# Optimization experiments

Measured on AMD Instinct MI355X. Metric: run time of the kernel, lower is better.

Reference implementation:

```python
import jax, jax.numpy as jnp
import numpy as np

B = 4096        # batch_size
H = 512         # hidden_rep_dim
S = 16384       # codebook_size (sae_dim)
K = 32          # opt.k (live topk per sample, applied batch-wise)
DEAD_K = 16     # opt.dead_k
DEAD_THRESH = 5


def setup_inputs() -> dict:
    key = jax.random.key(0)
    k0, k1, k2, k3 = jax.random.split(key, 4)
    x = jax.random.normal(k0, (B, H), dtype=jnp.float32)
    W1 = jax.random.normal(k1, (S, H), dtype=jnp.float32) * 0.02
    b1 = jnp.zeros((S,), dtype=jnp.float32)
    W2 = jax.random.normal(k2, (H, S), dtype=jnp.float32) * 0.02
    b2 = jnp.zeros((H,), dtype=jnp.float32)
    dead_features = jax.random.randint(k3, (S,), 0, 10, dtype=jnp.int32)
    return {"x": x, "W1": W1, "b1": b1, "W2": W2, "b2": b2,
            "dead_features": dead_features}


def reference(x, W1, b1, W2, b2, dead_features):
    Bn = x.shape[0]
    # _x = x - sae2.bias; f = relu(sae1(_x))
    f = jax.nn.relu((x - b2) @ W1.T + b1)          # [B, S]
    f_flat = f.reshape(-1)                          # [B*S]

    # batch topk over the flattened activations
    topk_vals, topk_inds = jax.lax.top_k(f_flat, K * Bn)

    # dead-feature masked activations; topk over them.
    # torch uses n = min(num_dead_slots, DEAD_K*B); taking a fixed DEAD_K*B topk
    # is value-equivalent since extra picks are zeros scattered onto zeros.
    dead_mask = (dead_features >= DEAD_THRESH)      # [S]
    dead_f_flat = jnp.where(
        jnp.broadcast_to(dead_mask[None, :], f.shape).reshape(-1),
        f_flat, jnp.zeros((), f.dtype))
    dead_vals, dead_inds = jax.lax.top_k(dead_f_flat, DEAD_K * Bn)

    # scatter kept values into zeroed tensors, unflatten
    f_sparse = jnp.zeros_like(f_flat).at[topk_inds].set(topk_vals).reshape(Bn, -1)
    dead_sparse = jnp.zeros_like(f_flat).at[dead_inds].set(dead_vals).reshape(Bn, -1)

    # dual decode through sae2
    x_rec = f_sparse @ W2.T + b2                    # [B, H]
    dead_x = dead_sparse @ W2.T + b2                # [B, H]
    return (x_rec, f_sparse, dead_x)
```

## Files before the change

### kernel.cpp

```cpp
#include <hip/hip_runtime.h>
#include <stdint.h>

#define B_  4096
#define H_  512
#define S_  16384
#define KT_ 16
#define NEED_MAIN 131072
#define NEED_DEAD 65536
#define DEAD_THRESH 5

#define T_LO 1.05078125f
#define BIN_BASE 0x3F800000u
#define BIN_SHIFT 13
#define NBIN 2048
#define REG_W 8
#define PAD_BINS 2
#define NSUB 8192
#define TIECAP 512

#define NSEG 16384
#define CAPSEG_M 128
#define CAPSEG_D 64
#define BNDCAP 16384
#define CAPROW_M 192
#define CAPROW_D 128

typedef __bf16 bf16x8 __attribute__((ext_vector_type(8)));
typedef float f32x4 __attribute__((ext_vector_type(4)));
typedef unsigned short ushort8 __attribute__((ext_vector_type(8)));

__device__ __forceinline__ uint32_t binOf(float v) {
    uint32_t b = (__float_as_uint(v) - BIN_BASE) >> BIN_SHIFT;
    return b > (NBIN - 1) ? (NBIN - 1) : b;
}
__device__ __forceinline__ uint16_t f2bf(float f) {
    uint32_t u = __float_as_uint(f);
    uint32_t r = u + 0x7FFFu + ((u >> 16) & 1u);
    return (uint16_t)(r >> 16);
}
__device__ __forceinline__ float bf2f(uint16_t b) {
    return __uint_as_float((uint32_t)b << 16);
}
__device__ __forceinline__ void gload16(const void* g, void* l) {
    __builtin_amdgcn_global_load_lds((const __attribute__((address_space(1))) uint32_t*)g,
                                     (__attribute__((address_space(3))) uint32_t*)l, 16, 0, 0);
}

__global__ __launch_bounds__(256) void transpose_k(const float* __restrict__ W2,
                                                   uint16_t* __restrict__ W2T) {
    __shared__ float tile[32][33];
    int s0 = blockIdx.x * 32, h0 = blockIdx.y * 32;
    int tx = threadIdx.x & 31, ty = threadIdx.x >> 5;
#pragma unroll
    for (int i = 0; i < 4; i++) {
        int h = h0 + ty + i * 8;
        tile[ty + i * 8][tx] = W2[(size_t)h * S_ + s0 + tx];
    }
    __syncthreads();
#pragma unroll
    for (int i = 0; i < 4; i++) {
        int s = s0 + ty + i * 8;
        W2T[(size_t)s * H_ + h0 + tx] = f2bf(tile[tx][ty + i * 8]);
    }
}

__global__ __launch_bounds__(256) void split_k(const float* __restrict__ src,
                                               const float* __restrict__ sub,
                                               uint8_t* __restrict__ Th,
                                               uint8_t* __restrict__ Tl) {
    int tid = blockIdx.x * 256 + threadIdx.x;
    int r = tid >> 6, h8 = tid & 63;
    int k0 = h8 << 3;
    const float* s = src + (size_t)r * H_ + k0;
    float4 v0 = *(const float4*)s, v1 = *(const float4*)(s + 4);
    float a[8] = {v0.x, v0.y, v0.z, v0.w, v1.x, v1.y, v1.z, v1.w};
    if (sub) {
        float4 c0 = *(const float4*)(sub + k0), c1 = *(const float4*)(sub + k0 + 4);
        a[0] -= c0.x; a[1] -= c0.y; a[2] -= c0.z; a[3] -= c0.w;
        a[4] -= c1.x; a[5] -= c1.y; a[6] -= c1.z; a[7] -= c1.w;
    }
    ushort8 Hh, Ll;
#pragma unroll
    for (int e = 0; e < 8; e++) {
        uint16_t h = f2bf(a[e]);
        Hh[e] = h;
        Ll[e] = f2bf(a[e] - bf2f(h));
    }
    int rb = r >> 7, kt = k0 >> 5;
    int mf = (r >> 4) & 7;
    int ln = (r & 15) | (((k0 >> 3) & 3) << 4);
    size_t byte = ((size_t)rb * KT_ + kt) * 8192 + (size_t)mf * 1024 + (size_t)ln * 16;
    *(ushort8*)(Th + byte) = Hh;
    if (Tl) *(ushort8*)(Tl + byte) = Ll;
}

__global__ __launch_bounds__(256) void gemm_fused(const uint8_t* __restrict__ AhT,
                                                  const uint8_t* __restrict__ AlT,
                                                  const uint8_t* __restrict__ WhT,
                                                  const float* __restrict__ b1,
                                                  const int* __restrict__ deadf,
                                                  uint2* __restrict__ glM,
                                                  uint2* __restrict__ glD,
                                                  uint32_t* __restrict__ bcM,
                                                  uint32_t* __restrict__ bcD,
                                                  float* __restrict__ fsp) {
    __shared__ uint8_t lds[2][3][8192];
    const int tid = threadIdx.x;
    const int lane = tid & 63, w = tid >> 6;
    const int wr = w >> 1, wc = w & 1;
    const int lin = blockIdx.y * 512 + blockIdx.x;
    const int xcd = lin & 7, idx = lin >> 3;
    const int mb = xcd * 4 + (idx & 3), nb = idx >> 2;

    const uint8_t* gAh = AhT + (size_t)mb * KT_ * 8192;
    const uint8_t* gAl = AlT + (size_t)mb * KT_ * 8192;
    const uint8_t* gBh = WhT + (size_t)nb * KT_ * 8192;

    f32x4 acc[4][4];
#pragma unroll
    for (int i = 0; i < 4; i++)
#pragma unroll
        for (int j = 0; j < 4; j++) acc[i][j] = (f32x4){0.f, 0.f, 0.f, 0.f};

    auto stage = [&](int buf, int kt) {
        size_t tb = (size_t)kt * 8192;
#pragma unroll
        for (int j = 0; j < 2; j++) {
            int off = j * 4096 + tid * 16;
            gload16(gAh + tb + off, &lds[buf][0][off]);
            gload16(gAl + tb + off, &lds[buf][1][off]);
            gload16(gBh + tb + off, &lds[buf][2][off]);
        }
    };

    float* Fb = fsp + (size_t)(mb * 128) * S_ + nb * 128;
    const int zc4 = (tid & 31) * 4, zr0 = tid >> 5;
    const float4 zf4 = {0.f, 0.f, 0.f, 0.f};

    stage(0, 0);
    __syncthreads();
    for (int kt = 0; kt < KT_; kt++) {
        int cur = kt & 1;
        if (kt + 1 < KT_) stage(cur ^ 1, kt + 1);
        *(float4*)(Fb + (size_t)(zr0 + kt * 8) * S_ + zc4) = zf4;
        bf16x8 ah[4], al[4], bh[4];
#pragma unroll
        for (int i = 0; i < 4; i++) {
            int offA = (wr * 4 + i) * 1024 + lane * 16;
            int offB = (wc * 4 + i) * 1024 + lane * 16;
            ah[i] = *(const bf16x8*)&lds[cur][0][offA];
            al[i] = *(const bf16x8*)&lds[cur][1][offA];
            bh[i] = *(const bf16x8*)&lds[cur][2][offB];
        }
#pragma unroll
        for (int i = 0; i < 4; i++)
#pragma unroll
            for (int j = 0; j < 4; j++)
                acc[i][j] = __builtin_amdgcn_mfma_f32_16x16x32_bf16(ah[i], bh[j], acc[i][j], 0, 0, 0);
#pragma unroll
        for (int i = 0; i < 4; i++)
#pragma unroll
            for (int j = 0; j < 4; j++)
                acc[i][j] = __builtin_amdgcn_mfma_f32_16x16x32_bf16(al[i], bh[j], acc[i][j], 0, 0, 0);
        __syncthreads();
    }

    const int col0 = nb * 128 + wc * 64 + (lane & 15);
    const int row0 = mb * 128 + wr * 64 + (lane >> 4) * 4;
    float b1v[4];
    int dd[4];
#pragma unroll
    for (int j = 0; j < 4; j++) {
        b1v[j] = b1[col0 + j * 16];
        dd[j] = (deadf[col0 + j * 16] >= DEAD_THRESH) ? 1 : 0;
    }
    const uint32_t gseg = (uint32_t)(mb * 128 + nb) * 4 + w;
    uint2* segM = glM + (size_t)gseg * CAPSEG_M;
    uint2* segD = glD + (size_t)gseg * CAPSEG_D;
    const uint64_t lmlt = ((uint64_t)1 << lane) - 1;
    uint32_t runM = 0, runD = 0;
#pragma unroll
    for (int i = 0; i < 4; i++)
#pragma unroll
        for (int j = 0; j < 4; j++)
#pragma unroll
            for (int r = 0; r < 4; r++) {
                float v = fmaxf(acc[i][j][r] + b1v[j], 0.0f);
                bool pass = v >= T_LO;
                uint64_t mask = __ballot(pass);
                if (mask) {
                    uint32_t prefix = (uint32_t)__popcll(mask & lmlt);
                    uint2 ent;
                    ent.x = (uint32_t)(row0 + i * 16 + r) * S_ + (uint32_t)(col0 + j * 16);
                    ent.y = __float_as_uint(v);
                    if (pass && runM + prefix < CAPSEG_M) segM[runM + prefix] = ent;
                    runM += (uint32_t)__popcll(mask);
                    bool dp = pass && dd[j];
                    uint64_t dmask = __ballot(dp);
                    if (dmask) {
                        uint32_t dprefix = (uint32_t)__popcll(dmask & lmlt);
                        if (dp && runD + dprefix < CAPSEG_D) segD[runD + dprefix] = ent;
                        runD += (uint32_t)__popcll(dmask);
                    }
                }
            }
    if (lane == 0) {
        bcM[gseg] = runM < CAPSEG_M ? runM : CAPSEG_M;
        bcD[gseg] = runD < CAPSEG_D ? runD : CAPSEG_D;
    }
}

__global__ __launch_bounds__(256) void seg_scan_k(const uint32_t* __restrict__ bcM,
                                                  const uint32_t* __restrict__ bcD,
                                                  uint32_t* __restrict__ soM,
                                                  uint32_t* __restrict__ soD,
                                                  uint32_t* __restrict__ cnts) {
    __shared__ uint32_t part[256];
    const int t = threadIdx.x;
    for (int sel = 0; sel < 2; sel++) {
        const uint32_t* bc = sel ? bcD : bcM;
        uint32_t* so = sel ? soD : soM;
        uint32_t s = 0;
        for (int i = 0; i < NSEG / 256; i++) s += bc[t * (NSEG / 256) + i];
        part[t] = s;
        __syncthreads();
        for (int d = 1; d < 256; d <<= 1) {
            uint32_t v = (t >= d) ? part[t - d] : 0;
            __syncthreads();
            part[t] += v;
            __syncthreads();
        }
        uint32_t run = (t == 0) ? 0 : part[t - 1];
        for (int i = 0; i < NSEG / 256; i++) {
            uint32_t c = bc[t * (NSEG / 256) + i];
            so[t * (NSEG / 256) + i] = run;
            run += c;
        }
        if (t == 255) cnts[sel] = run;
        __syncthreads();
    }
}

__global__ __launch_bounds__(256) void compact_hist_k(const uint2* __restrict__ glM,
                                                      const uint2* __restrict__ glD,
                                                      const uint32_t* __restrict__ bcM,
                                                      const uint32_t* __restrict__ bcD,
                                                      const uint32_t* __restrict__ soM,
                                                      const uint32_t* __restrict__ soD,
                                                      uint2* __restrict__ cmpM,
                                                      uint2* __restrict__ cmpD,
                                                      uint32_t* __restrict__ ghM,
                                                      uint32_t* __restrict__ ghD) {
    __shared__ uint32_t h[NBIN];
    int sel = blockIdx.y;
    const uint2* list = sel ? glD : glM;
    const uint32_t* bc = sel ? bcD : bcM;
    const uint32_t* so = sel ? soD : soM;
    uint2* cmp = sel ? cmpD : cmpM;
    uint32_t cap = sel ? CAPSEG_D : CAPSEG_M;
    uint32_t* gh = sel ? ghD : ghM;
    for (int i = threadIdx.x; i < NBIN; i += 256) h[i] = 0;
    __syncthreads();
    const int wv = threadIdx.x >> 6, lane = threadIdx.x & 63;
    for (uint32_t seg = blockIdx.x * 4 + wv; seg < NSEG; seg += gridDim.x * 4) {
        uint32_t n = bc[seg], off = so[seg];
        for (uint32_t i = lane; i < n; i += 64) {
            uint2 e = list[(size_t)seg * cap + i];
            cmp[off + i] = e;
            atomicAdd(&h[binOf(__uint_as_float(e.y))], 1u);
        }
    }
    __syncthreads();
    for (int i = threadIdx.x; i < NBIN; i += 256)
        if (h[i]) atomicAdd(&gh[i], h[i]);
}

__global__ __launch_bounds__(256) void scan_k(const uint32_t* __restrict__ ghM,
                                              const uint32_t* __restrict__ ghD,
                                              uint32_t* __restrict__ scal) {
    __shared__ uint32_t h[NBIN];
    __shared__ uint32_t csum[64];
    for (int sel = 0; sel < 2; sel++) {
        const uint32_t* gh = sel ? ghD : ghM;
        uint32_t need = sel ? NEED_DEAD : NEED_MAIN;
        for (int i = threadIdx.x; i < NBIN; i += 256) h[i] = gh[i];
        __syncthreads();
        if (threadIdx.x < 64) {
            uint32_t s = 0;
#pragma unroll
            for (int j = 0; j < 32; j++) s += h[threadIdx.x * 32 + j];
            csum[threadIdx.x] = s;
        }
        __syncthreads();
        if (threadIdx.x == 0) {
            uint32_t cum = 0; int c = 63;
            for (; c > 0; c--) { uint32_t cc = csum[c]; if (cum + cc >= need) break; cum += cc; }
            int b = c * 32 + 31;
            for (; b > c * 32; b--) { uint32_t cc = h[b]; if (cum + cc >= need) break; cum += cc; }
            uint32_t extra = 0;
            for (int j = b + 1; j < b + REG_W && j < NBIN; j++) extra += h[j];
            scal[sel ? 2 : 0] = (uint32_t)b;
            scal[sel ? 3 : 1] = need - cum + extra;
        }
        __syncthreads();
    }
}

__global__ __launch_bounds__(256) void bnd_filter_k(const uint2* __restrict__ cmpM,
                                                    const uint2* __restrict__ cmpD,
                                                    const uint32_t* __restrict__ scal,
                                                    uint2* __restrict__ bndM,
                                                    uint2* __restrict__ bndD,
                                                    uint32_t* __restrict__ cnts) {
    int sel = blockIdx.y;
    const uint2* list = sel ? cmpD : cmpM;
    uint2* bnd = sel ? bndD : bndM;
    uint32_t n = cnts[sel];
    uint32_t bs = scal[sel ? 2 : 0];
    for (uint32_t i = blockIdx.x * 256 + threadIdx.x; i < n; i += gridDim.x * 256) {
        uint2 ent = list[i];
        uint32_t bb = binOf(__uint_as_float(ent.y));
        if (bb + REG_W >= bs && bb <= bs + REG_W - 1) {
            uint32_t p = atomicAdd(&cnts[2 + sel], 1u);
            if (p < BNDCAP) bnd[p] = ent;
        }
    }
}

__global__ __launch_bounds__(256) void bnd_f64_k(const uint2* __restrict__ bndM,
                                                 const uint2* __restrict__ bndD,
                                                 const uint32_t* __restrict__ cnts,
                                                 const float* __restrict__ x,
                                                 const float* __restrict__ w1,
                                                 const float* __restrict__ b1,
                                                 const float* __restrict__ b2,
                                                 double* __restrict__ bvM,
                                                 double* __restrict__ bvD) {
    int sel = blockIdx.y;
    const uint2* bnd = sel ? bndD : bndM;
    double* bv64 = sel ? bvD : bvM;
    uint32_t n = cnts[2 + sel]; if (n > BNDCAP) n = BNDCAP;
    uint32_t i = blockIdx.x * 4 + (threadIdx.x >> 6);
    if (i >= n) return;
    const int lane = threadIdx.x & 63;
    uint2 ent = bnd[i];
    uint32_t m = ent.x >> 14, s = ent.x & (S_ - 1);
    const float* xr = x + (size_t)m * H_;
    const float* wr = w1 + (size_t)s * H_;
    double sum = 0.0;
#pragma unroll
    for (int e = 0; e < 8; e++) {
        int k = lane + e * 64;
        sum += ((double)xr[k] - (double)b2[k]) * (double)wr[k];
    }
#pragma unroll
    for (int off = 32; off; off >>= 1) sum += __shfl_down(sum, off, 64);
    if (lane == 0) {
        double tot = sum + (double)b1[s];
        bv64[i] = tot > 0.0 ? tot : 0.0;
    }
}

__global__ __launch_bounds__(1024) void rank_hist_k(const uint2* __restrict__ bndM,
                                                    const double* __restrict__ bvM,
                                                    const uint2* __restrict__ bndD,
                                                    const double* __restrict__ bvD,
                                                    uint32_t* __restrict__ cnts,
                                                    const uint32_t* __restrict__ scal,
                                                    uint2* __restrict__ exM,
                                                    uint2* __restrict__ exD) {
    int sel = blockIdx.x;
    const uint2* bnd = sel ? bndD : bndM;
    const double* bv = sel ? bvD : bvM;
    uint2* ex = sel ? exD : exM;
    uint32_t n = cnts[2 + sel]; if (n > BNDCAP) n = BNDCAP;
    uint32_t r = scal[sel ? 3 : 1]; if (r > n) r = n;
    uint32_t bs = scal[sel ? 2 : 0];
    uint32_t loBin = bs - (REG_W + PAD_BINS);
    uint32_t hiBin = bs + (REG_W + PAD_BINS);
    double lo = (double)__uint_as_float(BIN_BASE + (loBin << BIN_SHIFT));
    double hi = (double)__uint_as_float(BIN_BASE + (hiBin << BIN_SHIFT));
    double scale = (double)NSUB / (hi - lo);

    __shared__ uint32_t h[NSUB];
    __shared__ uint32_t cs[1024];
    __shared__ uint32_t c2[64];
    __shared__ uint32_t sCb, sAbove, sExPos, sTieCnt;
    __shared__ double tieV[TIECAP];
    __shared__ uint2 tieE[TIECAP];
    const int t = threadIdx.x;
    for (int i = t; i < NSUB; i += 1024) h[i] = 0;
    if (t == 0) { sExPos = 0; sTieCnt = 0; }
    __syncthreads();
    for (uint32_t i = t; i < n; i += 1024) {
        double v = bv[i];
        int k = (int)((v - lo) * scale);
        k = k < 0 ? 0 : (k > NSUB - 1 ? NSUB - 1 : k);
        atomicAdd(&h[k], 1u);
    }
    __syncthreads();
    {
        uint32_t s = 0;
#pragma unroll
        for (int j = 0; j < 8; j++) s += h[t * 8 + j];
        cs[t] = s;
    }
    __syncthreads();
    if (t < 64) {
        uint32_t s = 0;
#pragma unroll
        for (int j = 0; j < 16; j++) s += cs[t * 16 + j];
        c2[t] = s;
    }
    __syncthreads();
    if (t == 0) {
        uint32_t cum = 0; int w2 = 63;
        for (; w2 > 0; w2--) { if (cum + c2[w2] >= r) break; cum += c2[w2]; }
        int c = w2 * 16 + 15;
        for (; c > w2 * 16; c--) { if (cum + cs[c] >= r) break; cum += cs[c]; }
        int b = c * 8 + 7;
        for (; b > c * 8; b--) { if (cum + h[b] >= r) break; cum += h[b]; }
        sCb = (uint32_t)b;
        sAbove = cum;
    }
    __syncthreads();
    const uint32_t cb = sCb;
    uint32_t rr = r - sAbove;
    const int lane = t & 63;
    const uint64_t lmlt = ((uint64_t)1 << lane) - 1;
    for (uint32_t i0 = 0; i0 < n; i0 += 1024) {
        uint32_t i = i0 + t;
        bool valid = i < n;
        double v = valid ? bv[i] : -1.0;
        uint32_t k = 0;
        if (valid) {
            int kk = (int)((v - lo) * scale);
            k = (uint32_t)(kk < 0 ? 0 : (kk > NSUB - 1 ? NSUB - 1 : kk));
        }
        bool pick = valid && k > cb;
        uint64_t m = __ballot(pick);
        if (m) {
            uint32_t base = 0;
            if (lane == 0) base = atomicAdd(&sExPos, (uint32_t)__popcll(m));
            base = __shfl(base, 0, 64);
            if (pick) ex[base + __popcll(m & lmlt)] = bnd[i];
        }
        bool tie = valid && k == cb;
        uint64_t tm = __ballot(tie);
        if (tm) {
            uint32_t base = 0;
            if (lane == 0) base = atomicAdd(&sTieCnt, (uint32_t)__popcll(tm));
            base = __shfl(base, 0, 64);
            if (tie) {
                uint32_t p = base + __popcll(tm & lmlt);
                if (p < TIECAP) { tieV[p] = v; tieE[p] = bnd[i]; }
            }
        }
    }
    __syncthreads();
    uint32_t tc = sTieCnt; if (tc > TIECAP) tc = TIECAP;
    if (rr > tc) rr = tc;
    if (t < (int)tc) {
        double vi = tieV[t]; uint32_t ii = tieE[t].x;
        uint32_t rank = 0;
        for (uint32_t j = 0; j < tc; j++) {
            double vj = tieV[j]; uint32_t ij = tieE[j].x;
            rank += (vj > vi || (vj == vi && ij < ii)) ? 1u : 0u;
        }
        if (rank < rr) {
            uint32_t p = atomicAdd(&sExPos, 1u);
            ex[p] = tieE[t];
        }
    }
    __syncthreads();
    if (t == 0) cnts[4 + sel] = sExPos;
}

__global__ __launch_bounds__(256) void scatter_list_k(const uint2* __restrict__ cmpM,
                                                      const uint2* __restrict__ cmpD,
                                                      const uint32_t* __restrict__ cnts,
                                                      const uint32_t* __restrict__ scal,
                                                      float* __restrict__ fsp,
                                                      uint2* __restrict__ entM,
                                                      uint2* __restrict__ entD,
                                                      uint32_t* __restrict__ rcM,
                                                      uint32_t* __restrict__ rcD) {
    int sel = blockIdx.y;
    const uint2* list = sel ? cmpD : cmpM;
    uint2* entries = sel ? entD : entM;
    uint32_t* rowCnt = sel ? rcD : rcM;
    int capRow = sel ? CAPROW_D : CAPROW_M;
    uint32_t n = cnts[sel];
    uint32_t bsReg = scal[sel ? 2 : 0] + REG_W - 1;
    for (uint32_t i = blockIdx.x * 256 + threadIdx.x; i < n; i += gridDim.x * 256) {
        uint2 ent = list[i];
        float v = __uint_as_float(ent.y);
        if (binOf(v) <= bsReg) continue;
        if (!sel) fsp[ent.x] = v;
        uint32_t row = ent.x >> 14;
        uint32_t slot = atomicAdd(&rowCnt[row], 1u);
        if (slot < (uint32_t)capRow)
            entries[(size_t)row * capRow + slot] = make_uint2(ent.x & (S_ - 1), ent.y);
    }
}

__global__ __launch_bounds__(256) void scatter_ex_k(const uint2* __restrict__ exM,
                                                    const uint2* __restrict__ exD,
                                                    const uint32_t* __restrict__ cnts,
                                                    float* __restrict__ fsp,
                                                    uint2* __restrict__ entM,
                                                    uint2* __restrict__ entD,
                                                    uint32_t* __restrict__ rcM,
                                                    uint32_t* __restrict__ rcD) {
    int sel = blockIdx.y;
    const uint2* arr = sel ? exD : exM;
    uint2* entries = sel ? entD : entM;
    uint32_t* rowCnt = sel ? rcD : rcM;
    int capRow = sel ? CAPROW_D : CAPROW_M;
    uint32_t n = cnts[4 + sel]; if (n > BNDCAP) n = BNDCAP;
    uint32_t i = blockIdx.x * 256 + threadIdx.x;
    if (i >= n) return;
    uint2 ent = arr[i];
    float v = __uint_as_float(ent.y);
    if (!sel) fsp[ent.x] = v;
    uint32_t row = ent.x >> 14;
    uint32_t slot = atomicAdd(&rowCnt[row], 1u);
    if (slot < (uint32_t)capRow)
        entries[(size_t)row * capRow + slot] = make_uint2(ent.x & (S_ - 1), ent.y);
}

__global__ __launch_bounds__(512) void decode_k(const uint2* __restrict__ entM,
                                                const uint32_t* __restrict__ rcM,
                                                const uint2* __restrict__ entD,
                                                const uint32_t* __restrict__ rcD,
                                                const uint16_t* __restrict__ W2T,
                                                const float* __restrict__ b2,
                                                float* __restrict__ xrec,
                                                float* __restrict__ deadx) {
    __shared__ uint2 em[CAPROW_M];
    __shared__ uint2 ed[CAPROW_D];
    int b = blockIdx.x, h = threadIdx.x;
    uint32_t nm = rcM[b]; if (nm > CAPROW_M) nm = CAPROW_M;
    uint32_t nd = rcD[b]; if (nd > CAPROW_D) nd = CAPROW_D;
    for (uint32_t i = h; i < nm; i += 512) em[i] = entM[(size_t)b * CAPROW_M + i];
    for (uint32_t i = h; i < nd; i += 512) ed[i] = entD[(size_t)b * CAPROW_D + i];
    __syncthreads();
    float bias = b2[h];
    float a = bias, d = bias;
    for (uint32_t i = 0; i < nm; i++)
        a = fmaf(__uint_as_float(em[i].y), bf2f(W2T[(size_t)em[i].x * H_ + h]), a);
    for (uint32_t i = 0; i < nd; i++)
        d = fmaf(__uint_as_float(ed[i].y), bf2f(W2T[(size_t)ed[i].x * H_ + h]), d);
    xrec[(size_t)b * H_ + h] = a;
    deadx[(size_t)b * H_ + h] = d;
}

extern "C" void kernel_launch(void* const* d_in, const int* in_sizes, int n_in,
                              void* d_out, int out_size, void* d_ws, size_t ws_size,
                              hipStream_t stream) {
    const float* x = (const float*)d_in[0];
    const float* w1 = (const float*)d_in[1];
    const float* b1 = (const float*)d_in[2];
    const float* w2 = (const float*)d_in[3];
    const float* b2 = (const float*)d_in[4];
    const int* deadf = (const int*)d_in[5];

    float* out = (float*)d_out;
    float* xrec = out;
    float* fsp = out + (size_t)B_ * H_;
    float* deadx = out + (size_t)B_ * H_ + (size_t)B_ * S_;

    uint8_t* w = (uint8_t*)d_ws;
    size_t off = 0;
    auto alloc = [&](size_t bytes) { uint8_t* p = w + off; off = (off + bytes + 255) & ~(size_t)255; return p; };

    uint16_t* W2T = (uint16_t*)alloc((size_t)S_ * H_ * 2);
    uint8_t* ctrl = alloc(NBIN * 8 + 128 + (size_t)B_ * 8);
    uint32_t* ghM = (uint32_t*)ctrl;
    uint32_t* ghD = (uint32_t*)(ctrl + NBIN * 4);
    uint32_t* cnts = (uint32_t*)(ctrl + NBIN * 8);
    uint32_t* scal = (uint32_t*)(ctrl + NBIN * 8 + 64);
    uint32_t* rcM = (uint32_t*)(ctrl + NBIN * 8 + 128);
    uint32_t* rcD = (uint32_t*)(ctrl + NBIN * 8 + 128 + B_ * 4);
    size_t ctrlBytes = NBIN * 8 + 128 + (size_t)B_ * 8;

    uint2* listM = (uint2*)alloc((size_t)NSEG * CAPSEG_M * 8);
    uint2* listD = (uint2*)alloc((size_t)NSEG * CAPSEG_D * 8);
    uint32_t* bcM = (uint32_t*)alloc((size_t)NSEG * 4);
    uint32_t* bcD = (uint32_t*)alloc((size_t)NSEG * 4);
    uint32_t* soM = (uint32_t*)alloc((size_t)NSEG * 4);
    uint32_t* soD = (uint32_t*)alloc((size_t)NSEG * 4);
    uint2* cmpM = (uint2*)alloc((size_t)NSEG * CAPSEG_M * 8);
    uint2* cmpD = (uint2*)alloc((size_t)NSEG * CAPSEG_D * 8);
    uint2* bndM = (uint2*)alloc((size_t)BNDCAP * 8);
    uint2* bndD = (uint2*)alloc((size_t)BNDCAP * 8);
    double* bvM = (double*)alloc((size_t)BNDCAP * 8);
    double* bvD = (double*)alloc((size_t)BNDCAP * 8);
    uint2* exM = (uint2*)alloc((size_t)BNDCAP * 8);
    uint2* exD = (uint2*)alloc((size_t)BNDCAP * 8);
    uint2* entM = (uint2*)alloc((size_t)B_ * CAPROW_M * 8);
    uint2* entD = (uint2*)alloc((size_t)B_ * CAPROW_D * 8);
    uint8_t* AhT = alloc((size_t)B_ * H_ * 2);
    uint8_t* AlT = alloc((size_t)B_ * H_ * 2);
    uint8_t* WhT = alloc((size_t)S_ * H_ * 2);

    (void)hipMemsetAsync(ctrl, 0, ctrlBytes, stream);
    transpose_k<<<dim3(S_ / 32, H_ / 32), 256, 0, stream>>>(w2, W2T);
    split_k<<<(B_ * 64) / 256, 256, 0, stream>>>(x, b2, AhT, AlT);
    split_k<<<(S_ * 64) / 256, 256, 0, stream>>>(w1, nullptr, WhT, nullptr);
    gemm_fused<<<dim3(512, 8), 256, 0, stream>>>(AhT, AlT, WhT, b1, deadf,
                                                 listM, listD, bcM, bcD, fsp);
    seg_scan_k<<<1, 256, 0, stream>>>(bcM, bcD, soM, soD, cnts);
    compact_hist_k<<<dim3(256, 2), 256, 0, stream>>>(listM, listD, bcM, bcD, soM, soD,
                                                     cmpM, cmpD, ghM, ghD);
    scan_k<<<1, 256, 0, stream>>>(ghM, ghD, scal);
    bnd_filter_k<<<dim3(1024, 2), 256, 0, stream>>>(cmpM, cmpD, scal, bndM, bndD, cnts);
    bnd_f64_k<<<dim3(BNDCAP / 4, 2), 256, 0, stream>>>(bndM, bndD, cnts, x, w1, b1, b2, bvM, bvD);
    rank_hist_k<<<2, 1024, 0, stream>>>(bndM, bvM, bndD, bvD, cnts, scal, exM, exD);
    scatter_list_k<<<dim3(1024, 2), 256, 0, stream>>>(cmpM, cmpD, cnts, scal, fsp,
                                                      entM, entD, rcM, rcD);
    scatter_ex_k<<<dim3(BNDCAP / 256, 2), 256, 0, stream>>>(exM, exD, cnts, fsp, entM, entD, rcM, rcD);
    decode_k<<<B_, 512, 0, stream>>>(entM, rcM, entD, rcD, W2T, b2, xrec, deadx);
}
```

Before: 494.1 us.

## Fuse split, boundary filter/f64, and exact scatter kernels; widen GEMM to 8 waves

Merges the two split launches into one grid, fuses the boundary filter with the fp64 recompute, and folds the exact-tie scatter into rank_hist so the ex buffers and the scatter_ex launch go away. The GEMM block grows to 512 threads with each wave covering a 64x32 sub-tile, which doubles the number of per-wave candidate segments (NSEG raised to match). The intent is fewer launches and more waves for latency hiding. The cost is fewer accumulators per wave, less register-level reuse of the A fragments, and fp64 work done serially per wave inside the ballot loop.

```diff
diff --git a/kernel.cpp b/kernel.cpp
--- a/kernel.cpp
+++ b/kernel.cpp
@@ -18,7 +18,7 @@
 #define NSUB 8192
 #define TIECAP 512
 
-#define NSEG 16384
+#define NSEG 32768
 #define CAPSEG_M 128
 #define CAPSEG_D 64
 #define BNDCAP 16384
@@ -64,18 +64,22 @@
     }
 }
 
-__global__ __launch_bounds__(256) void split_k(const float* __restrict__ src,
-                                               const float* __restrict__ sub,
-                                               uint8_t* __restrict__ Th,
-                                               uint8_t* __restrict__ Tl) {
-    int tid = blockIdx.x * 256 + threadIdx.x;
+__global__ __launch_bounds__(256) void split_all_k(const float* __restrict__ x,
+                                                   const float* __restrict__ w1,
+                                                   const float* __restrict__ b2,
+                                                   uint8_t* __restrict__ AhT,
+                                                   uint8_t* __restrict__ AlT,
+                                                   uint8_t* __restrict__ WhT) {
+    int isX = blockIdx.x < 1024;
+    int tid = (isX ? blockIdx.x : blockIdx.x - 1024) * 256 + threadIdx.x;
     int r = tid >> 6, h8 = tid & 63;
     int k0 = h8 << 3;
+    const float* src = isX ? x : w1;
     const float* s = src + (size_t)r * H_ + k0;
     float4 v0 = *(const float4*)s, v1 = *(const float4*)(s + 4);
     float a[8] = {v0.x, v0.y, v0.z, v0.w, v1.x, v1.y, v1.z, v1.w};
-    if (sub) {
-        float4 c0 = *(const float4*)(sub + k0), c1 = *(const float4*)(sub + k0 + 4);
+    if (isX) {
+        float4 c0 = *(const float4*)(b2 + k0), c1 = *(const float4*)(b2 + k0 + 4);
         a[0] -= c0.x; a[1] -= c0.y; a[2] -= c0.z; a[3] -= c0.w;
         a[4] -= c1.x; a[5] -= c1.y; a[6] -= c1.z; a[7] -= c1.w;
     }
@@ -90,11 +94,15 @@
     int mf = (r >> 4) & 7;
     int ln = (r & 15) | (((k0 >> 3) & 3) << 4);
     size_t byte = ((size_t)rb * KT_ + kt) * 8192 + (size_t)mf * 1024 + (size_t)ln * 16;
-    *(ushort8*)(Th + byte) = Hh;
-    if (Tl) *(ushort8*)(Tl + byte) = Ll;
-}
-
-__global__ __launch_bounds__(256) void gemm_fused(const uint8_t* __restrict__ AhT,
+    if (isX) {
+        *(ushort8*)(AhT + byte) = Hh;
+        *(ushort8*)(AlT + byte) = Ll;
+    } else {
+        *(ushort8*)(WhT + byte) = Hh;
+    }
+}
+
+__global__ __launch_bounds__(512) void gemm_fused(const uint8_t* __restrict__ AhT,
                                                   const uint8_t* __restrict__ AlT,
                                                   const uint8_t* __restrict__ WhT,
                                                   const float* __restrict__ b1,
@@ -107,7 +115,7 @@
     __shared__ uint8_t lds[2][3][8192];
     const int tid = threadIdx.x;
     const int lane = tid & 63, w = tid >> 6;
-    const int wr = w >> 1, wc = w & 1;
+    const int wr = w >> 2, wc = w & 3;
     const int lin = blockIdx.y * 512 + blockIdx.x;
     const int xcd = lin & 7, idx = lin >> 3;
     const int mb = xcd * 4 + (idx & 3), nb = idx >> 2;
@@ -116,21 +124,18 @@
     const uint8_t* gAl = AlT + (size_t)mb * KT_ * 8192;
     const uint8_t* gBh = WhT + (size_t)nb * KT_ * 8192;
 
-    f32x4 acc[4][4];
+    f32x4 acc[4][2];
 #pragma unroll
     for (int i = 0; i < 4; i++)
 #pragma unroll
-        for (int j = 0; j < 4; j++) acc[i][j] = (f32x4){0.f, 0.f, 0.f, 0.f};
+        for (int j = 0; j < 2; j++) acc[i][j] = (f32x4){0.f, 0.f, 0.f, 0.f};
 
     auto stage = [&](int buf, int kt) {
         size_t tb = (size_t)kt * 8192;
-#pragma unroll
-        for (int j = 0; j < 2; j++) {
-            int off = j * 4096 + tid * 16;
-            gload16(gAh + tb + off, &lds[buf][0][off]);
-            gload16(gAl + tb + off, &lds[buf][1][off]);
-            gload16(gBh + tb + off, &lds[buf][2][off]);
-        }
+        int o = tid * 16;
+        gload16(gAh + tb + o, &lds[buf][0][o]);
+        gload16(gAl + tb + o, &lds[buf][1][o]);
+        gload16(gBh + tb + o, &lds[buf][2][o]);
     };
 
     float* Fb = fsp + (size_t)(mb * 128) * S_ + nb * 128;
@@ -142,39 +147,42 @@
     for (int kt = 0; kt < KT_; kt++) {
         int cur = kt & 1;
         if (kt + 1 < KT_) stage(cur ^ 1, kt + 1);
-        *(float4*)(Fb + (size_t)(zr0 + kt * 8) * S_ + zc4) = zf4;
-        bf16x8 ah[4], al[4], bh[4];
+        if (kt < 8) *(float4*)(Fb + (size_t)(zr0 + kt * 16) * S_ + zc4) = zf4;
+        bf16x8 ah[4], al[4], bh[2];
 #pragma unroll
         for (int i = 0; i < 4; i++) {
             int offA = (wr * 4 + i) * 1024 + lane * 16;
-            int offB = (wc * 4 + i) * 1024 + lane * 16;
             ah[i] = *(const bf16x8*)&lds[cur][0][offA];
             al[i] = *(const bf16x8*)&lds[cur][1][offA];
-            bh[i] = *(const bf16x8*)&lds[cur][2][offB];
+        }
+#pragma unroll
+        for (int j = 0; j < 2; j++) {
+            int offB = (wc * 2 + j) * 1024 + lane * 16;
+            bh[j] = *(const bf16x8*)&lds[cur][2][offB];
         }
 #pragma unroll
         for (int i = 0; i < 4; i++)
 #pragma unroll
-            for (int j = 0; j < 4; j++)
+            for (int j = 0; j < 2; j++)
                 acc[i][j] = __builtin_amdgcn_mfma_f32_16x16x32_bf16(ah[i], bh[j], acc[i][j], 0, 0, 0);
 #pragma unroll
         for (int i = 0; i < 4; i++)
 #pragma unroll
-            for (int j = 0; j < 4; j++)
+            for (int j = 0; j < 2; j++)
                 acc[i][j] = __builtin_amdgcn_mfma_f32_16x16x32_bf16(al[i], bh[j], acc[i][j], 0, 0, 0);
         __syncthreads();
     }
 
-    const int col0 = nb * 128 + wc * 64 + (lane & 15);
+    const int col0 = nb * 128 + wc * 32 + (lane & 15);
     const int row0 = mb * 128 + wr * 64 + (lane >> 4) * 4;
-    float b1v[4];
-    int dd[4];
-#pragma unroll
-    for (int j = 0; j < 4; j++) {
+    float b1v[2];
+    int dd[2];
+#pragma unroll
+    for (int j = 0; j < 2; j++) {
         b1v[j] = b1[col0 + j * 16];
         dd[j] = (deadf[col0 + j * 16] >= DEAD_THRESH) ? 1 : 0;
     }
-    const uint32_t gseg = (uint32_t)(mb * 128 + nb) * 4 + w;
+    const uint32_t gseg = (uint32_t)(mb * 128 + nb) * 8 + w;
     uint2* segM = glM + (size_t)gseg * CAPSEG_M;
     uint2* segD = glD + (size_t)gseg * CAPSEG_D;
     const uint64_t lmlt = ((uint64_t)1 << lane) - 1;
@@ -182,7 +190,7 @@
 #pragma unroll
     for (int i = 0; i < 4; i++)
 #pragma unroll
-        for (int j = 0; j < 4; j++)
+        for (int j = 0; j < 2; j++)
 #pragma unroll
             for (int r = 0; r < 4; r++) {
                 float v = fmaxf(acc[i][j][r] + b1v[j], 0.0f);
@@ -306,58 +314,62 @@
     }
 }
 
-__global__ __launch_bounds__(256) void bnd_filter_k(const uint2* __restrict__ cmpM,
-                                                    const uint2* __restrict__ cmpD,
-                                                    const uint32_t* __restrict__ scal,
-                                                    uint2* __restrict__ bndM,
-                                                    uint2* __restrict__ bndD,
-                                                    uint32_t* __restrict__ cnts) {
+__global__ __launch_bounds__(256) void bnd_fused_k(const uint2* __restrict__ cmpM,
+                                                   const uint2* __restrict__ cmpD,
+                                                   const uint32_t* __restrict__ scal,
+                                                   const float* __restrict__ x,
+                                                   const float* __restrict__ w1,
+                                                   const float* __restrict__ b1,
+                                                   const float* __restrict__ b2,
+                                                   uint2* __restrict__ bndM,
+                                                   uint2* __restrict__ bndD,
+                                                   double* __restrict__ bvM,
+                                                   double* __restrict__ bvD,
+                                                   uint32_t* __restrict__ cnts) {
     int sel = blockIdx.y;
     const uint2* list = sel ? cmpD : cmpM;
     uint2* bnd = sel ? bndD : bndM;
+    double* bv64 = sel ? bvD : bvM;
     uint32_t n = cnts[sel];
     uint32_t bs = scal[sel ? 2 : 0];
-    for (uint32_t i = blockIdx.x * 256 + threadIdx.x; i < n; i += gridDim.x * 256) {
-        uint2 ent = list[i];
-        uint32_t bb = binOf(__uint_as_float(ent.y));
-        if (bb + REG_W >= bs && bb <= bs + REG_W - 1) {
-            uint32_t p = atomicAdd(&cnts[2 + sel], 1u);
-            if (p < BNDCAP) bnd[p] = ent;
-        }
-    }
-}
-
-__global__ __launch_bounds__(256) void bnd_f64_k(const uint2* __restrict__ bndM,
-                                                 const uint2* __restrict__ bndD,
-                                                 const uint32_t* __restrict__ cnts,
-                                                 const float* __restrict__ x,
-                                                 const float* __restrict__ w1,
-                                                 const float* __restrict__ b1,
-                                                 const float* __restrict__ b2,
-                                                 double* __restrict__ bvM,
-                                                 double* __restrict__ bvD) {
-    int sel = blockIdx.y;
-    const uint2* bnd = sel ? bndD : bndM;
-    double* bv64 = sel ? bvD : bvM;
-    uint32_t n = cnts[2 + sel]; if (n > BNDCAP) n = BNDCAP;
-    uint32_t i = blockIdx.x * 4 + (threadIdx.x >> 6);
-    if (i >= n) return;
-    const int lane = threadIdx.x & 63;
-    uint2 ent = bnd[i];
-    uint32_t m = ent.x >> 14, s = ent.x & (S_ - 1);
-    const float* xr = x + (size_t)m * H_;
-    const float* wr = w1 + (size_t)s * H_;
-    double sum = 0.0;
-#pragma unroll
-    for (int e = 0; e < 8; e++) {
-        int k = lane + e * 64;
-        sum += ((double)xr[k] - (double)b2[k]) * (double)wr[k];
-    }
-#pragma unroll
-    for (int off = 32; off; off >>= 1) sum += __shfl_down(sum, off, 64);
-    if (lane == 0) {
-        double tot = sum + (double)b1[s];
-        bv64[i] = tot > 0.0 ? tot : 0.0;
+    const int lane = threadIdx.x & 63, wv = threadIdx.x >> 6;
+    const uint32_t stride = gridDim.x * 4 * 64;
+    for (uint32_t base = (blockIdx.x * 4 + wv) * 64; base < n; base += stride) {
+        uint32_t i = base + lane;
+        uint2 ent = make_uint2(0u, 0u);
+        bool pass = false;
+        if (i < n) {
+            ent = list[i];
+            uint32_t bb = binOf(__uint_as_float(ent.y));
+            pass = (bb + REG_W >= bs) && (bb <= bs + REG_W - 1);
+        }
+        uint64_t mm = __ballot(pass);
+        while (mm) {
+            int b = __ffsll((unsigned long long)mm) - 1;
+            mm &= mm - 1;
+            uint32_t ex_ = __shfl(ent.x, b, 64);
+            uint32_t ey_ = __shfl(ent.y, b, 64);
+            uint32_t pos = 0;
+            if (lane == 0) pos = atomicAdd(&cnts[2 + sel], 1u);
+            pos = __shfl(pos, 0, 64);
+            if (pos >= BNDCAP) continue;
+            uint32_t m = ex_ >> 14, s = ex_ & (S_ - 1);
+            const float* xr = x + (size_t)m * H_;
+            const float* wr = w1 + (size_t)s * H_;
+            double sum = 0.0;
+#pragma unroll
+            for (int e = 0; e < 8; e++) {
+                int k = lane + e * 64;
+                sum += ((double)xr[k] - (double)b2[k]) * (double)wr[k];
+            }
+#pragma unroll
+            for (int off = 32; off; off >>= 1) sum += __shfl_down(sum, off, 64);
+            if (lane == 0) {
+                double tot = sum + (double)b1[s];
+                bv64[pos] = tot > 0.0 ? tot : 0.0;
+                bnd[pos] = make_uint2(ex_, ey_);
+            }
+        }
     }
 }
 
@@ -367,12 +379,17 @@
                                                     const double* __restrict__ bvD,
                                                     uint32_t* __restrict__ cnts,
                                                     const uint32_t* __restrict__ scal,
-                                                    uint2* __restrict__ exM,
-                                                    uint2* __restrict__ exD) {
+                                                    float* __restrict__ fsp,
+                                                    uint2* __restrict__ entM,
+                                                    uint2* __restrict__ entD,
+                                                    uint32_t* __restrict__ rcM,
+                                                    uint32_t* __restrict__ rcD) {
     int sel = blockIdx.x;
     const uint2* bnd = sel ? bndD : bndM;
     const double* bv = sel ? bvD : bvM;
-    uint2* ex = sel ? exD : exM;
+    uint2* entries = sel ? entD : entM;
+    uint32_t* rowCnt = sel ? rcD : rcM;
+    const int capRow = sel ? CAPROW_D : CAPROW_M;
     uint32_t n = cnts[2 + sel]; if (n > BNDCAP) n = BNDCAP;
     uint32_t r = scal[sel ? 3 : 1]; if (r > n) r = n;
     uint32_t bs = scal[sel ? 2 : 0];
@@ -385,12 +402,12 @@
     __shared__ uint32_t h[NSUB];
     __shared__ uint32_t cs[1024];
     __shared__ uint32_t c2[64];
-    __shared__ uint32_t sCb, sAbove, sExPos, sTieCnt;
+    __shared__ uint32_t sCb, sAbove, sTieCnt;
     __shared__ double tieV[TIECAP];
     __shared__ uint2 tieE[TIECAP];
     const int t = threadIdx.x;
     for (int i = t; i < NSUB; i += 1024) h[i] = 0;
-    if (t == 0) { sExPos = 0; sTieCnt = 0; }
+    if (t == 0) sTieCnt = 0;
     __syncthreads();
     for (uint32_t i = t; i < n; i += 1024) {
         double v = bv[i];
@@ -437,13 +454,14 @@
             int kk = (int)((v - lo) * scale);
             k = (uint32_t)(kk < 0 ? 0 : (kk > NSUB - 1 ? NSUB - 1 : kk));
         }
-        bool pick = valid && k > cb;
-        uint64_t m = __ballot(pick);
-        if (m) {
-            uint32_t base = 0;
-            if (lane == 0) base = atomicAdd(&sExPos, (uint32_t)__popcll(m));
-            base = __shfl(base, 0, 64);
-            if (pick) ex[base + __popcll(m & lmlt)] = bnd[i];
+        if (valid && k > cb) {
+            uint2 ent = bnd[i];
+            float fv = __uint_as_float(ent.y);
+            if (!sel) fsp[ent.x] = fv;
+            uint32_t row = ent.x >> 14;
+            uint32_t slot = atomicAdd(&rowCnt[row], 1u);
+            if (slot < (uint32_t)capRow)
+                entries[(size_t)row * capRow + slot] = make_uint2(ent.x & (S_ - 1), ent.y);
         }
         bool tie = valid && k == cb;
         uint64_t tm = __ballot(tie);
@@ -468,12 +486,15 @@
             rank += (vj > vi || (vj == vi && ij < ii)) ? 1u : 0u;
         }
         if (rank < rr) {
-            uint32_t p = atomicAdd(&sExPos, 1u);
-            ex[p] = tieE[t];
-        }
-    }
-    __syncthreads();
-    if (t == 0) cnts[4 + sel] = sExPos;
+            uint2 ent = tieE[t];
+            float fv = __uint_as_float(ent.y);
+            if (!sel) fsp[ent.x] = fv;
+            uint32_t row = ent.x >> 14;
+            uint32_t slot = atomicAdd(&rowCnt[row], 1u);
+            if (slot < (uint32_t)capRow)
+                entries[(size_t)row * capRow + slot] = make_uint2(ent.x & (S_ - 1), ent.y);
+        }
+    }
 }
 
 __global__ __launch_bounds__(256) void scatter_list_k(const uint2* __restrict__ cmpM,
@@ -504,31 +525,6 @@
     }
 }
 
-__global__ __launch_bounds__(256) void scatter_ex_k(const uint2* __restrict__ exM,
-                                                    const uint2* __restrict__ exD,
-                                                    const uint32_t* __restrict__ cnts,
-                                                    float* __restrict__ fsp,
-                                                    uint2* __restrict__ entM,
-                                                    uint2* __restrict__ entD,
-                                                    uint32_t* __restrict__ rcM,
-                                                    uint32_t* __restrict__ rcD) {
-    int sel = blockIdx.y;
-    const uint2* arr = sel ? exD : exM;
-    uint2* entries = sel ? entD : entM;
-    uint32_t* rowCnt = sel ? rcD : rcM;
-    int capRow = sel ? CAPROW_D : CAPROW_M;
-    uint32_t n = cnts[4 + sel]; if (n > BNDCAP) n = BNDCAP;
-    uint32_t i = blockIdx.x * 256 + threadIdx.x;
-    if (i >= n) return;
-    uint2 ent = arr[i];
-    float v = __uint_as_float(ent.y);
-    if (!sel) fsp[ent.x] = v;
-    uint32_t row = ent.x >> 14;
-    uint32_t slot = atomicAdd(&rowCnt[row], 1u);
-    if (slot < (uint32_t)capRow)
-        entries[(size_t)row * capRow + slot] = make_uint2(ent.x & (S_ - 1), ent.y);
-}
-
 __global__ __launch_bounds__(512) void decode_k(const uint2* __restrict__ entM,
                                                 const uint32_t* __restrict__ rcM,
                                                 const uint2* __restrict__ entD,
@@ -596,8 +592,6 @@
     uint2* bndD = (uint2*)alloc((size_t)BNDCAP * 8);
     double* bvM = (double*)alloc((size_t)BNDCAP * 8);
     double* bvD = (double*)alloc((size_t)BNDCAP * 8);
-    uint2* exM = (uint2*)alloc((size_t)BNDCAP * 8);
-    uint2* exD = (uint2*)alloc((size_t)BNDCAP * 8);
     uint2* entM = (uint2*)alloc((size_t)B_ * CAPROW_M * 8);
     uint2* entD = (uint2*)alloc((size_t)B_ * CAPROW_D * 8);
     uint8_t* AhT = alloc((size_t)B_ * H_ * 2);
@@ -606,19 +600,18 @@
 
     (void)hipMemsetAsync(ctrl, 0, ctrlBytes, stream);
     transpose_k<<<dim3(S_ / 32, H_ / 32), 256, 0, stream>>>(w2, W2T);
-    split_k<<<(B_ * 64) / 256, 256, 0, stream>>>(x, b2, AhT, AlT);
-    split_k<<<(S_ * 64) / 256, 256, 0, stream>>>(w1, nullptr, WhT, nullptr);
-    gemm_fused<<<dim3(512, 8), 256, 0, stream>>>(AhT, AlT, WhT, b1, deadf,
+    split_all_k<<<5120, 256, 0, stream>>>(x, w1, b2, AhT, AlT, WhT);
+    gemm_fused<<<dim3(512, 8), 512, 0, stream>>>(AhT, AlT, WhT, b1, deadf,
                                                  listM, listD, bcM, bcD, fsp);
     seg_scan_k<<<1, 256, 0, stream>>>(bcM, bcD, soM, soD, cnts);
     compact_hist_k<<<dim3(256, 2), 256, 0, stream>>>(listM, listD, bcM, bcD, soM, soD,
                                                      cmpM, cmpD, ghM, ghD);
     scan_k<<<1, 256, 0, stream>>>(ghM, ghD, scal);
-    bnd_filter_k<<<dim3(1024, 2), 256, 0, stream>>>(cmpM, cmpD, scal, bndM, bndD, cnts);
-    bnd_f64_k<<<dim3(BNDCAP / 4, 2), 256, 0, stream>>>(bndM, bndD, cnts, x, w1, b1, b2, bvM, bvD);
-    rank_hist_k<<<2, 1024, 0, stream>>>(bndM, bvM, bndD, bvD, cnts, scal, exM, exD);
+    bnd_fused_k<<<dim3(1024, 2), 256, 0, stream>>>(cmpM, cmpD, scal, x, w1, b1, b2,
+                                                   bndM, bndD, bvM, bvD, cnts);
+    rank_hist_k<<<2, 1024, 0, stream>>>(bndM, bvM, bndD, bvD, cnts, scal,
+                                        fsp, entM, entD, rcM, rcD);
     scatter_list_k<<<dim3(1024, 2), 256, 0, stream>>>(cmpM, cmpD, cnts, scal, fsp,
                                                       entM, entD, rcM, rcD);
-    scatter_ex_k<<<dim3(BNDCAP / 256, 2), 256, 0, stream>>>(exM, exD, cnts, fsp, entM, entD, rcM, rcD);
     decode_k<<<B_, 512, 0, stream>>>(entM, rcM, entD, rcD, W2T, b2, xrec, deadx);
 }
```

Result: slower. 634.8 us (+28.5%).
